# Optimization experiments

Hardware: AMD Instinct MI355X
Metric: run time of the kernel (lower is better)

Reference implementation:

```python
import jax, jax.numpy as jnp
import numpy as np

B, L, V, H = 2, 2048, 1024, 16
HD = V // H  # head size 64
EPS = 1e-3   # keras LayerNormalization default


def setup_inputs() -> dict:
    key = jax.random.key(0)
    ks = jax.random.split(key, 10)
    scale = 1.0 / np.sqrt(V)
    return {
        "query": jax.random.normal(ks[0], (B, L, V), jnp.float32),
        "key_t": jax.random.normal(ks[1], (B, L, V), jnp.float32),
        "value": jax.random.normal(ks[2], (B, L, V), jnp.float32),
        "Wq": jax.random.normal(ks[3], (H, V, HD), jnp.float32) * scale,
        "Wk": jax.random.normal(ks[4], (H, V, HD), jnp.float32) * scale,
        "Wv": jax.random.normal(ks[5], (H, V, HD), jnp.float32) * scale,
        "gamma": jnp.ones((V,), jnp.float32),
        "beta": jnp.zeros((V,), jnp.float32),
        "query_mask": jax.random.randint(ks[6], (B, L), 0, 2, jnp.int32),
        "value_mask": jax.random.randint(ks[7], (B, L), 0, 2, jnp.int32),
    }


def reference(query, key_t, value, Wq, Wk, Wv, gamma, beta, query_mask, value_mask):
    qm = query_mask.astype(jnp.float32)  # (B,L)
    vm = value_mask.astype(jnp.float32)  # (B,L)

    # per-head no-bias Dense projections, batched over heads
    Q = jnp.einsum('blv,hvd->bhld', query, Wq)
    K = jnp.einsum('blv,hvd->bhld', key_t, Wk)
    Vh = jnp.einsum('blv,hvd->bhld', value, Wv)

    scores = jnp.einsum('bhld,bhmd->bhlm', Q, K) / jnp.sqrt(jnp.float32(HD))
    attn = jax.nn.softmax(scores, axis=-1)

    # post-softmax multiplicative masking (faithful to original)
    tri = jnp.tril(jnp.ones((L, L), jnp.float32))  # (L,L) causal
    attn = attn * tri[None, None, :, :]
    attn = attn * qm[:, None, :, None] * vm[:, None, None, :]

    heads = jnp.einsum('bhlm,bhmd->bhld', attn, Vh)
    x = heads.transpose(0, 2, 1, 3).reshape(B, L, V)  # concat heads

    # dropout is identity at inference
    y = x + query
    mu = jnp.mean(y, axis=-1, keepdims=True)
    var = jnp.mean((y - mu) ** 2, axis=-1, keepdims=True)
    return gamma * (y - mu) * jax.lax.rsqrt(var + EPS) + beta
```

## Files before the change

### kernel.cpp

```cpp
#include <hip/hip_runtime.h>
#include <math.h>

constexpr int NB = 2;
constexpr int SL = 2048;
constexpr int NV = 1024;
constexpr int NH = 16;
constexpr int DH = 64;
constexpr float LN_EPS = 1e-3f;

typedef __bf16 bf16_t;
typedef __bf16 v8bf __attribute__((ext_vector_type(8)));
typedef float  v4f  __attribute__((ext_vector_type(4)));

__device__ __forceinline__ unsigned pack_bf16(float a, float b) {
  unsigned short ua = __builtin_bit_cast(unsigned short, (bf16_t)a);
  unsigned short ub = __builtin_bit_cast(unsigned short, (bf16_t)b);
  return (unsigned)ua | ((unsigned)ub << 16);
}
__device__ __forceinline__ void async_cp16(const void* g, void* l) {
  __builtin_amdgcn_global_load_lds(
      (const __attribute__((address_space(1))) unsigned int*)g,
      (__attribute__((address_space(3))) unsigned int*)l, 16, 0, 0);
}
__device__ __forceinline__ void drain_dma() {
  asm volatile("s_waitcnt vmcnt(0)" ::: "memory");
}

__global__ __launch_bounds__(256)
void acvt(const float* __restrict__ q, const float* __restrict__ k,
          const float* __restrict__ v, bf16_t* __restrict__ oq,
          bf16_t* __restrict__ ok, bf16_t* __restrict__ ov) {
  const int z = blockIdx.y;
  const float* src = z == 0 ? q : (z == 1 ? k : v);
  bf16_t*      dst = z == 0 ? oq : (z == 1 ? ok : ov);
  const size_t i = ((size_t)blockIdx.x * 256 + threadIdx.x) * 4;
  float4 f = *(const float4*)(src + i);
  uint2 u = {pack_bf16(f.x, f.y), pack_bf16(f.z, f.w)};
  *(uint2*)(dst + i) = u;
}

__global__ __launch_bounds__(256)
void wcvt(const float* __restrict__ Wq, const float* __restrict__ Wk,
          const float* __restrict__ Wv, bf16_t* __restrict__ Wt) {
  __shared__ float ls[64][65];
  const int z = blockIdx.z;
  const float* W = z == 0 ? Wq : (z == 1 ? Wk : Wv);
  const float sc = z == 0 ? 0.125f * 1.44269504f : 1.0f;
  const int h = blockIdx.y, v0 = blockIdx.x * 64;
  const int t = threadIdx.x;
  const int rr = t >> 4, c4 = t & 15;
  const float* src = W + ((size_t)h * NV + v0) * DH;
#pragma unroll
  for (int it = 0; it < 4; ++it) {
    float4 f = *(const float4*)(src + (size_t)(rr + it * 16) * DH + c4 * 4);
    ls[rr + it * 16][c4 * 4 + 0] = f.x;
    ls[rr + it * 16][c4 * 4 + 1] = f.y;
    ls[rr + it * 16][c4 * 4 + 2] = f.z;
    ls[rr + it * 16][c4 * 4 + 3] = f.w;
  }
  __syncthreads();
  const int dd = t >> 2, vq = t & 3;
  bf16_t tmp[16];
#pragma unroll
  for (int i = 0; i < 16; ++i) tmp[i] = (bf16_t)(ls[vq * 16 + i][dd] * sc);
  bf16_t* dst = Wt + ((size_t)z * NV + h * 64 + dd) * NV + v0 + vq * 16;
  *(v8bf*)dst = *(v8bf*)&tmp[0];
  *(v8bf*)(dst + 8) = *(v8bf*)&tmp[8];
}

__global__ __launch_bounds__(256, 4)
void proj_mfma(const bf16_t* __restrict__ A0, const bf16_t* __restrict__ A1,
               const bf16_t* __restrict__ A2, const bf16_t* __restrict__ Wtb,
               const int* __restrict__ vmask,
               bf16_t* __restrict__ O0, bf16_t* __restrict__ O1,
               bf16_t* __restrict__ O2) {
  __shared__ __align__(16) bf16_t Asb[2][128 * 32];
  __shared__ __align__(16) bf16_t Wsb[2][128 * 32];

  const int z = blockIdx.z;
  const bf16_t* A   = z == 0 ? A0 : (z == 1 ? A1 : A2);
  bf16_t*       out = z == 0 ? O0 : (z == 1 ? O1 : O2);
  const bf16_t* W   = Wtb + (size_t)z * NV * NV;

  const int t = threadIdx.x, w = t >> 6, lane = t & 63;
  const int g = lane >> 4, lx = lane & 15;
  const int m0 = blockIdx.x * 128, n0 = blockIdx.y * 128;
  const int rbase = (w >> 1) * 64, cbase = (w & 1) * 64;

  const int sr = lane >> 2;
  const int sc = (lane & 3);
  auto stageA = [&](int k0, int buf) {
#pragma unroll
    for (int s = 0; s < 2; ++s) {
      const int r = w * 32 + s * 16 + sr;
      const int c = sc ^ (r & 3);
      async_cp16(A + (size_t)(m0 + r) * NV + k0 + c * 8,
                 (char*)Asb[buf] + (w * 32 + s * 16) * 64);
    }
  };
  auto stageW = [&](int k0, int buf) {
#pragma unroll
    for (int s = 0; s < 2; ++s) {
      const int r = w * 32 + s * 16 + sr;
      const int c = sc ^ (r & 3);
      async_cp16(W + (size_t)(n0 + r) * NV + k0 + c * 8,
                 (char*)Wsb[buf] + (w * 32 + s * 16) * 64);
    }
  };

  v4f acc[4][4] = {};
  stageA(0, 0);
  stageW(0, 0);

  for (int it = 0; it < 32; ++it) {
    const int buf = it & 1;
    drain_dma();
    __syncthreads();
    if (it < 31) {
      stageA((it + 1) * 32, buf ^ 1);
      stageW((it + 1) * 32, buf ^ 1);
    }
    v8bf af[4], wf[4];
#pragma unroll
    for (int rt = 0; rt < 4; ++rt) {
      const int row = rbase + rt * 16 + lx;
      af[rt] = *(const v8bf*)((const char*)Asb[buf] + row * 64 +
                              ((g ^ (row & 3)) * 16));
    }
#pragma unroll
    for (int ct = 0; ct < 4; ++ct) {
      const int row = cbase + ct * 16 + lx;
      wf[ct] = *(const v8bf*)((const char*)Wsb[buf] + row * 64 +
                              ((g ^ (row & 3)) * 16));
    }
#pragma unroll
    for (int rt = 0; rt < 4; ++rt)
#pragma unroll
      for (int ct = 0; ct < 4; ++ct)
        acc[rt][ct] = __builtin_amdgcn_mfma_f32_16x16x32_bf16(
            af[rt], wf[ct], acc[rt][ct], 0, 0, 0);
  }

  if (z < 2) {
#pragma unroll
    for (int rt = 0; rt < 4; ++rt) {
#pragma unroll
      for (int reg = 0; reg < 4; ++reg) {
        const int row = m0 + rbase + rt * 16 + g * 4 + reg;
        const int b = row >> 11, l = row & (SL - 1);
#pragma unroll
        for (int ct = 0; ct < 4; ++ct) {
          const int n = n0 + cbase + ct * 16 + lx;
          const int h = n >> 6, d = n & 63;
          out[((size_t)(b * NH + h) * SL + l) * DH + d] = (bf16_t)acc[rt][ct][reg];
        }
      }
    }
  } else {
#pragma unroll
    for (int rt = 0; rt < 4; ++rt) {
      const int row = m0 + rbase + rt * 16 + g * 4;
      const int b = row >> 11, l = row & (SL - 1);
      float vm0 = (float)vmask[b * SL + l + 0];
      float vm1 = (float)vmask[b * SL + l + 1];
      float vm2 = (float)vmask[b * SL + l + 2];
      float vm3 = (float)vmask[b * SL + l + 3];
#pragma unroll
      for (int ct = 0; ct < 4; ++ct) {
        const int n = n0 + cbase + ct * 16 + lx;
        const int h = n >> 6, d = n & 63;
        uint2 u = {pack_bf16(acc[rt][ct][0] * vm0, acc[rt][ct][1] * vm1),
                   pack_bf16(acc[rt][ct][2] * vm2, acc[rt][ct][3] * vm3)};
        *(uint2*)&out[((size_t)(b * NH + h) * DH + d) * SL + l] = u;
      }
    }
  }
}

__global__ __launch_bounds__(256, 4)
void attn_mfma(const bf16_t* __restrict__ Qg, const bf16_t* __restrict__ Kg,
               const bf16_t* __restrict__ Vtg_all, const int* __restrict__ qmask,
               float* __restrict__ Xout) {
  __shared__ __align__(16) bf16_t kbuf[2][64 * 64];
  __shared__ __align__(16) bf16_t vbuf[2][64 * 64];
  __shared__ __align__(16) bf16_t Ps[4][16 * 64];

  const int id = blockIdx.x;
  const int bh = (id & 7) | ((id >> 8) << 3);
  const int qraw = (id >> 3) & 31;
  const int qb = ((id >> 8) & 1) ? qraw : 31 - qraw;
  const int t = threadIdx.x, w = t >> 6, lane = t & 63;
  const int g = lane >> 4, lx = lane & 15;
  const int b = bh >> 4, h = bh & 15;
  const int l0 = qb * 64;
  const int lastAct = qb;

  const bf16_t* Kb  = Kg + (size_t)bh * SL * DH;
  const bf16_t* Vtg = Vtg_all + (size_t)bh * DH * SL;

  v8bf qf[2];
#pragma unroll
  for (int ks = 0; ks < 2; ++ks)
    qf[ks] = *(const v8bf*)&Qg[((size_t)bh * SL + l0 + w * 16 + lx) * DH +
                               ks * 32 + g * 8];

  v4f O[4] = {};
  float suml = 0.f;

  const int sr_off = lane >> 3, sc_l = lane & 7;
  auto stageK = [&](int mb, int buf) {
#pragma unroll
    for (int s = 0; s < 2; ++s) {
      const int r = w * 16 + s * 8 + sr_off;
      const int c = sc_l ^ (r & 7);
      async_cp16(Kb + (size_t)(mb + r) * DH + c * 8,
                 (char*)kbuf[buf] + (w * 16 + s * 8) * 128);
    }
  };
  auto stageV = [&](int mb, int buf) {
#pragma unroll
    for (int s = 0; s < 2; ++s) {
      const int r = w * 16 + s * 8 + sr_off;
      const int c = sc_l ^ (r & 7);
      async_cp16(Vtg + (size_t)r * SL + mb + c * 8,
                 (char*)vbuf[buf] + (w * 16 + s * 8) * 128);
    }
  };

  stageK(0, 0);
  stageV(0, 0);

  for (int mt = 0; mt <= lastAct; ++mt) {
    const int pb = mt & 1;
    drain_dma();
    __syncthreads();
    if (mt < SL / 64 - 1)  stageK((mt + 1) * 64, pb ^ 1);
    if (mt + 1 <= lastAct) stageV((mt + 1) * 64, pb ^ 1);

    v4f S[4];
#pragma unroll
    for (int mt2 = 0; mt2 < 4; ++mt2) S[mt2] = (v4f){0.f, 0.f, 0.f, 0.f};
#pragma unroll
    for (int ks = 0; ks < 2; ++ks)
#pragma unroll
      for (int mt2 = 0; mt2 < 4; ++mt2) {
        const int row = mt2 * 16 + lx;
        v8bf kf = *(const v8bf*)((const char*)kbuf[pb] + row * 128 +
                                 (((ks * 4 + g) ^ (lx & 7)) * 16));
        S[mt2] = __builtin_amdgcn_mfma_f32_16x16x32_bf16(kf, qf[ks], S[mt2],
                                                         0, 0, 0);
      }

    const bool diagzone = (mt == qb);
#pragma unroll
    for (int mt2 = 0; mt2 < 4; ++mt2) {
      float e0 = __builtin_amdgcn_exp2f(S[mt2][0]);
      float e1 = __builtin_amdgcn_exp2f(S[mt2][1]);
      float e2 = __builtin_amdgcn_exp2f(S[mt2][2]);
      float e3 = __builtin_amdgcn_exp2f(S[mt2][3]);
      suml += (e0 + e1) + (e2 + e3);
      if (diagzone) {
        const int ml = mt * 64 + mt2 * 16 + g * 4;
        const int ql = l0 + w * 16 + lx;
        e0 = (ml + 0 <= ql) ? e0 : 0.f;
        e1 = (ml + 1 <= ql) ? e1 : 0.f;
        e2 = (ml + 2 <= ql) ? e2 : 0.f;
        e3 = (ml + 3 <= ql) ? e3 : 0.f;
      }
      uint2 u = {pack_bf16(e0, e1), pack_bf16(e2, e3)};
      *(uint2*)((char*)Ps[w] + lx * 128 +
                ((mt2 * 32 + g * 8) ^ ((lx & 7) << 4))) = u;
    }

    __builtin_amdgcn_wave_barrier();

#pragma unroll
    for (int ks = 0; ks < 2; ++ks) {
      v8bf pf = *(const v8bf*)((const char*)Ps[w] + lx * 128 +
                               ((ks * 64 + g * 16) ^ ((lx & 7) << 4)));
#pragma unroll
      for (int dt = 0; dt < 4; ++dt) {
        const int row = dt * 16 + lx;
        v8bf vf = *(const v8bf*)((const char*)vbuf[pb] + row * 128 +
                                 (((ks * 4 + g) ^ (lx & 7)) * 16));
        O[dt] = __builtin_amdgcn_mfma_f32_16x16x32_bf16(pf, vf, O[dt],
                                                        0, 0, 0);
      }
    }
  }

  for (int mt = lastAct + 1; mt < SL / 64; ++mt) {
    const int pb = mt & 1;
    drain_dma();
    __syncthreads();
    if (mt < SL / 64 - 1) stageK((mt + 1) * 64, pb ^ 1);
    v4f S[4];
#pragma unroll
    for (int mt2 = 0; mt2 < 4; ++mt2) S[mt2] = (v4f){0.f, 0.f, 0.f, 0.f};
#pragma unroll
    for (int ks = 0; ks < 2; ++ks)
#pragma unroll
      for (int mt2 = 0; mt2 < 4; ++mt2) {
        const int row = mt2 * 16 + lx;
        v8bf kf = *(const v8bf*)((const char*)kbuf[pb] + row * 128 +
                                 (((ks * 4 + g) ^ (lx & 7)) * 16));
        S[mt2] = __builtin_amdgcn_mfma_f32_16x16x32_bf16(kf, qf[ks], S[mt2],
                                                         0, 0, 0);
      }
#pragma unroll
    for (int mt2 = 0; mt2 < 4; ++mt2)
      suml += (__builtin_amdgcn_exp2f(S[mt2][0]) +
               __builtin_amdgcn_exp2f(S[mt2][1])) +
              (__builtin_amdgcn_exp2f(S[mt2][2]) +
               __builtin_amdgcn_exp2f(S[mt2][3]));
  }

  suml += __shfl_xor(suml, 16);
  suml += __shfl_xor(suml, 32);
#pragma unroll
  for (int reg = 0; reg < 4; ++reg) {
    const int q = l0 + w * 16 + g * 4 + reg;
    const float den = __shfl(suml, g * 4 + reg);
    const float inv = (float)qmask[b * SL + q] / den;
#pragma unroll
    for (int dt = 0; dt < 4; ++dt)
      Xout[((size_t)(b * SL + q)) * NV + h * DH + dt * 16 + lx] =
          O[dt][reg] * inv;
  }
}

__global__ __launch_bounds__(256)
void ln_kernel(const float* __restrict__ X, const float* __restrict__ query,
               const float* __restrict__ gamma, const float* __restrict__ beta,
               float* __restrict__ out) {
  const int row = blockIdx.x * 4 + (threadIdx.x >> 6);
  const int lane = threadIdx.x & 63;
  const float* xr = X + (size_t)row * NV;
  const float* qr = query + (size_t)row * NV;
  float4 y[4];
  float s = 0.f, ss = 0.f;
#pragma unroll
  for (int i = 0; i < 4; ++i) {
    const int col = lane * 4 + i * 256;
    float4 xv = *(const float4*)(xr + col);
    float4 qv = *(const float4*)(qr + col);
    y[i].x = xv.x + qv.x; y[i].y = xv.y + qv.y;
    y[i].z = xv.z + qv.z; y[i].w = xv.w + qv.w;
    s  += (y[i].x + y[i].y) + (y[i].z + y[i].w);
    ss += (y[i].x * y[i].x + y[i].y * y[i].y) +
          (y[i].z * y[i].z + y[i].w * y[i].w);
  }
#pragma unroll
  for (int off = 1; off < 64; off <<= 1) {
    s  += __shfl_xor(s, off);
    ss += __shfl_xor(ss, off);
  }
  const float mu   = s * (1.f / NV);
  const float var  = ss * (1.f / NV) - mu * mu;
  const float rstd = rsqrtf(var + LN_EPS);
#pragma unroll
  for (int i = 0; i < 4; ++i) {
    const int col = lane * 4 + i * 256;
    float4 gv = *(const float4*)(gamma + col);
    float4 bv = *(const float4*)(beta + col);
    float4 o;
    o.x = gv.x * (y[i].x - mu) * rstd + bv.x;
    o.y = gv.y * (y[i].y - mu) * rstd + bv.y;
    o.z = gv.z * (y[i].z - mu) * rstd + bv.z;
    o.w = gv.w * (y[i].w - mu) * rstd + bv.w;
    *(float4*)(out + (size_t)row * NV + col) = o;
  }
}

extern "C" void kernel_launch(void* const* d_in, const int* in_sizes, int n_in,
                              void* d_out, int out_size, void* d_ws, size_t ws_size,
                              hipStream_t stream) {
  const float* query = (const float*)d_in[0];
  const float* key_t = (const float*)d_in[1];
  const float* value = (const float*)d_in[2];
  const float* Wq    = (const float*)d_in[3];
  const float* Wk    = (const float*)d_in[4];
  const float* Wv    = (const float*)d_in[5];
  const float* gamma = (const float*)d_in[6];
  const float* beta  = (const float*)d_in[7];
  const int*   qmask = (const int*)d_in[8];
  const int*   vmask = (const int*)d_in[9];
  float* out = (float*)d_out;

  const size_t per = (size_t)NB * NH * SL * DH;
  bf16_t* Qws = (bf16_t*)d_ws;
  bf16_t* Kws = Qws + per;
  bf16_t* Vws = Kws + per;
  bf16_t* Wtb = Vws + per;
  bf16_t* Aq  = Wtb + (size_t)3 * NV * NV;
  bf16_t* Ak  = Aq + per;
  bf16_t* Av  = Ak + per;

  acvt<<<dim3((NB * SL * NV) / (256 * 4), 3), 256, 0, stream>>>(
      query, key_t, value, Aq, Ak, Av);
  wcvt<<<dim3(16, 16, 3), 256, 0, stream>>>(Wq, Wk, Wv, Wtb);
  proj_mfma<<<dim3(32, 8, 3), 256, 0, stream>>>(Aq, Ak, Av, Wtb,
                                                vmask, Qws, Kws, Vws);
  attn_mfma<<<1024, 256, 0, stream>>>(Qws, Kws, Vws, qmask, out);
  ln_kernel<<<NB * SL / 4, 256, 0, stream>>>(out, query, gamma, beta, out);
}
```

Baseline: 205.6 us.

## Fuse activation bf16 conversion into projection GEMM and residual add into attention

Removes the standalone fp32-to-bf16 activation conversion kernel; the projection GEMM now DMA-stages fp32 tiles into LDS with a wider swizzle and packs to bf16 when loading MFMA fragments. The residual add of query moves into the attention epilogue, so the LayerNorm kernel no longer reads query. This cuts a kernel launch and a full write-and-reread of the converted activations. In exchange, LDS per block doubles for the A tile, the occupancy hint drops to 3, and conversion ALU work enters the GEMM inner loop.

```diff
diff --git a/kernel.cpp b/kernel.cpp
--- a/kernel.cpp
+++ b/kernel.cpp
@@ -24,19 +24,6 @@
 }
 __device__ __forceinline__ void drain_dma() {
   asm volatile("s_waitcnt vmcnt(0)" ::: "memory");
-}
-
-__global__ __launch_bounds__(256)
-void acvt(const float* __restrict__ q, const float* __restrict__ k,
-          const float* __restrict__ v, bf16_t* __restrict__ oq,
-          bf16_t* __restrict__ ok, bf16_t* __restrict__ ov) {
-  const int z = blockIdx.y;
-  const float* src = z == 0 ? q : (z == 1 ? k : v);
-  bf16_t*      dst = z == 0 ? oq : (z == 1 ? ok : ov);
-  const size_t i = ((size_t)blockIdx.x * 256 + threadIdx.x) * 4;
-  float4 f = *(const float4*)(src + i);
-  uint2 u = {pack_bf16(f.x, f.y), pack_bf16(f.z, f.w)};
-  *(uint2*)(dst + i) = u;
 }
 
 __global__ __launch_bounds__(256)
@@ -68,17 +55,17 @@
   *(v8bf*)(dst + 8) = *(v8bf*)&tmp[8];
 }
 
-__global__ __launch_bounds__(256, 4)
-void proj_mfma(const bf16_t* __restrict__ A0, const bf16_t* __restrict__ A1,
-               const bf16_t* __restrict__ A2, const bf16_t* __restrict__ Wtb,
+__global__ __launch_bounds__(256, 3)
+void proj_mfma(const float* __restrict__ A0, const float* __restrict__ A1,
+               const float* __restrict__ A2, const bf16_t* __restrict__ Wtb,
                const int* __restrict__ vmask,
                bf16_t* __restrict__ O0, bf16_t* __restrict__ O1,
                bf16_t* __restrict__ O2) {
-  __shared__ __align__(16) bf16_t Asb[2][128 * 32];
+  __shared__ __align__(16) float  Asb[2][128 * 32];
   __shared__ __align__(16) bf16_t Wsb[2][128 * 32];
 
   const int z = blockIdx.z;
-  const bf16_t* A   = z == 0 ? A0 : (z == 1 ? A1 : A2);
+  const float*  A   = z == 0 ? A0 : (z == 1 ? A1 : A2);
   bf16_t*       out = z == 0 ? O0 : (z == 1 ? O1 : O2);
   const bf16_t* W   = Wtb + (size_t)z * NV * NV;
 
@@ -87,17 +74,17 @@
   const int m0 = blockIdx.x * 128, n0 = blockIdx.y * 128;
   const int rbase = (w >> 1) * 64, cbase = (w & 1) * 64;
 
-  const int sr = lane >> 2;
-  const int sc = (lane & 3);
+  const int sr8 = lane >> 3, sc8 = lane & 7;
   auto stageA = [&](int k0, int buf) {
 #pragma unroll
-    for (int s = 0; s < 2; ++s) {
-      const int r = w * 32 + s * 16 + sr;
-      const int c = sc ^ (r & 3);
-      async_cp16(A + (size_t)(m0 + r) * NV + k0 + c * 8,
-                 (char*)Asb[buf] + (w * 32 + s * 16) * 64);
+    for (int s = 0; s < 4; ++s) {
+      const int r = w * 32 + s * 8 + sr8;
+      const int c = sc8 ^ (r & 7);
+      async_cp16(A + (size_t)(m0 + r) * NV + k0 + c * 4,
+                 (char*)Asb[buf] + (w * 32 + s * 8) * 128);
     }
   };
+  const int sr = lane >> 2, sc = lane & 3;
   auto stageW = [&](int k0, int buf) {
 #pragma unroll
     for (int s = 0; s < 2; ++s) {
@@ -124,8 +111,13 @@
 #pragma unroll
     for (int rt = 0; rt < 4; ++rt) {
       const int row = rbase + rt * 16 + lx;
-      af[rt] = *(const v8bf*)((const char*)Asb[buf] + row * 64 +
-                              ((g ^ (row & 3)) * 16));
+      const char* rb = (const char*)Asb[buf] + row * 128;
+      const int p0 = (2 * g) ^ (row & 7);
+      float4 fa = *(const float4*)(rb + p0 * 16);
+      float4 fb = *(const float4*)(rb + (p0 ^ 1) * 16);
+      uint4 u = {pack_bf16(fa.x, fa.y), pack_bf16(fa.z, fa.w),
+                 pack_bf16(fb.x, fb.y), pack_bf16(fb.z, fb.w)};
+      af[rt] = __builtin_bit_cast(v8bf, u);
     }
 #pragma unroll
     for (int ct = 0; ct < 4; ++ct) {
@@ -180,7 +172,7 @@
 __global__ __launch_bounds__(256, 4)
 void attn_mfma(const bf16_t* __restrict__ Qg, const bf16_t* __restrict__ Kg,
                const bf16_t* __restrict__ Vtg_all, const int* __restrict__ qmask,
-               float* __restrict__ Xout) {
+               const float* __restrict__ queryg, float* __restrict__ Xout) {
   __shared__ __align__(16) bf16_t kbuf[2][64 * 64];
   __shared__ __align__(16) bf16_t vbuf[2][64 * 64];
   __shared__ __align__(16) bf16_t Ps[4][16 * 64];
@@ -322,30 +314,27 @@
     const int q = l0 + w * 16 + g * 4 + reg;
     const float den = __shfl(suml, g * 4 + reg);
     const float inv = (float)qmask[b * SL + q] / den;
+    const size_t rowoff = ((size_t)(b * SL + q)) * NV + h * DH;
 #pragma unroll
     for (int dt = 0; dt < 4; ++dt)
-      Xout[((size_t)(b * SL + q)) * NV + h * DH + dt * 16 + lx] =
-          O[dt][reg] * inv;
+      Xout[rowoff + dt * 16 + lx] =
+          O[dt][reg] * inv + queryg[rowoff + dt * 16 + lx];
   }
 }
 
 __global__ __launch_bounds__(256)
-void ln_kernel(const float* __restrict__ X, const float* __restrict__ query,
+void ln_kernel(const float* __restrict__ X,
                const float* __restrict__ gamma, const float* __restrict__ beta,
                float* __restrict__ out) {
   const int row = blockIdx.x * 4 + (threadIdx.x >> 6);
   const int lane = threadIdx.x & 63;
   const float* xr = X + (size_t)row * NV;
-  const float* qr = query + (size_t)row * NV;
   float4 y[4];
   float s = 0.f, ss = 0.f;
 #pragma unroll
   for (int i = 0; i < 4; ++i) {
     const int col = lane * 4 + i * 256;
-    float4 xv = *(const float4*)(xr + col);
-    float4 qv = *(const float4*)(qr + col);
-    y[i].x = xv.x + qv.x; y[i].y = xv.y + qv.y;
-    y[i].z = xv.z + qv.z; y[i].w = xv.w + qv.w;
+    y[i] = *(const float4*)(xr + col);
     s  += (y[i].x + y[i].y) + (y[i].z + y[i].w);
     ss += (y[i].x * y[i].x + y[i].y * y[i].y) +
           (y[i].z * y[i].z + y[i].w * y[i].w);
@@ -392,15 +381,10 @@
   bf16_t* Kws = Qws + per;
   bf16_t* Vws = Kws + per;
   bf16_t* Wtb = Vws + per;
-  bf16_t* Aq  = Wtb + (size_t)3 * NV * NV;
-  bf16_t* Ak  = Aq + per;
-  bf16_t* Av  = Ak + per;
-
-  acvt<<<dim3((NB * SL * NV) / (256 * 4), 3), 256, 0, stream>>>(
-      query, key_t, value, Aq, Ak, Av);
+
   wcvt<<<dim3(16, 16, 3), 256, 0, stream>>>(Wq, Wk, Wv, Wtb);
-  proj_mfma<<<dim3(32, 8, 3), 256, 0, stream>>>(Aq, Ak, Av, Wtb,
+  proj_mfma<<<dim3(32, 8, 3), 256, 0, stream>>>(query, key_t, value, Wtb,
                                                 vmask, Qws, Kws, Vws);
-  attn_mfma<<<1024, 256, 0, stream>>>(Qws, Kws, Vws, qmask, out);
-  ln_kernel<<<NB * SL / 4, 256, 0, stream>>>(out, query, gamma, beta, out);
-}
+  attn_mfma<<<1024, 256, 0, stream>>>(Qws, Kws, Vws, qmask, query, out);
+  ln_kernel<<<NB * SL / 4, 256, 0, stream>>>(out, gamma, beta, out);
+}
```

Measured after the change: 217.6 us. 1.06x slower.
